# Kernel tuning notes

Measured on AMD Instinct MI355X. Metric: run time of the kernel, lower is better.

## Reference

```python
import jax, jax.numpy as jnp
import numpy as np

SIGMA = 1.0
LN2 = 0.6931471805599453


def _raster_mask(kd, kh, kw, include_center):
    # PixelCNN-style causal mask in (depth, h, w) raster order
    idx = np.arange(kd * kh * kw).reshape(kd, kh, kw)
    c = (kd * kh * kw) // 2
    m = (idx <= c) if include_center else (idx < c)
    return jnp.asarray(m, jnp.float32)[None, None]  # [1,1,kd,kh,kw] (OIDHW broadcast)


def _conv3d(x, w, b, padding):
    y = jax.lax.conv_general_dilated(x, w, (1, 1, 1), padding,
                                     dimension_numbers=('NCDHW', 'OIDHW', 'NCDHW'))
    return y + b[None, :, None, None, None]


def _quantize1d(x, centers):
    # distances of every element to every center: [..., L]
    d = (x[..., None] - centers) ** 2
    phi_soft = jax.nn.softmax(-SIGMA * d, axis=-1)
    qsoft = jnp.einsum('...l,l->...', phi_soft, centers)
    symbols = jnp.argmin(d, axis=-1)  # int32 hard assignment
    qhard = centers[symbols]
    return qsoft, qhard, symbols


def setup_inputs() -> dict:
    key = jax.random.key(0)
    ks = jax.random.split(key, 8)
    N, H, W, C = 4, 128, 128, 16
    K, L = 24, 6
    s = 0.05
    return {
        'x': jax.random.normal(ks[0], (N, H, W, C), jnp.float32),
        'centers': jax.random.uniform(ks[1], (L,), jnp.float32, -2.0, 2.0),
        'w0': jax.random.normal(ks[2], (K, 1, 3, 3, 3), jnp.float32) * s,
        'b0': jnp.zeros((K,), jnp.float32),
        'w1': jax.random.normal(ks[3], (K, K, 3, 3, 3), jnp.float32) * s,
        'b1': jnp.zeros((K,), jnp.float32),
        'w2': jax.random.normal(ks[4], (K, K, 3, 3, 3), jnp.float32) * s,
        'b2': jnp.zeros((K,), jnp.float32),
        'w_out': jax.random.normal(ks[5], (L, K, 1, 1, 1), jnp.float32) * s,
        'b_out': jnp.zeros((L,), jnp.float32),
    }


def reference(x, centers, w0, b0, w1, b1, w2, b2, w_out, b_out):
    # ---- soft/hard quantization with straight-through estimator ----
    qsoft, qhard, symbols = _quantize1d(x, centers)
    qbar = qsoft + jax.lax.stop_gradient(qhard - qsoft)  # [N,H,W,C] NHWC

    pc_in = jnp.transpose(qbar, (0, 3, 1, 2))[:, None]      # [N,1,C,H,W] (depth=C)
    tgt = jnp.transpose(symbols, (0, 3, 1, 2))              # [N,C,H,W]

    # pad input volume with pad_value = centers[0] (causal boundary symbol)
    pad_value = centers[0].astype(pc_in.dtype)
    v = jax.lax.pad(pc_in, pad_value,
                    [(0, 0, 0), (0, 0, 0), (1, 1, 0), (1, 1, 0), (1, 1, 0)])

    mask_a = _raster_mask(3, 3, 3, include_center=False)
    mask_b = _raster_mask(3, 3, 3, include_center=True)

    # res_shallow: masked-A conv -> masked-B conv -> masked-B conv + residual -> 1x1x1 logits
    h0 = jax.nn.relu(_conv3d(v, w0 * mask_a, b0, 'VALID'))     # [N,K,C,H,W]
    h1 = jax.nn.relu(_conv3d(h0, w1 * mask_b, b1, 'SAME'))
    h2 = _conv3d(h1, w2 * mask_b, b2, 'SAME') + h0
    logits = _conv3d(jax.nn.relu(h2), w_out, b_out, 'SAME')    # [N,L,C,H,W]

    # per-element bitcost: cross-entropy of hard symbols, in bits
    lp = jax.nn.log_softmax(logits, axis=1)
    bc = -jnp.take_along_axis(lp, tgt[:, None], axis=1)[:, 0] / LN2  # [N,C,H,W]
    bc_train = jnp.transpose(bc, (0, 2, 3, 1))                        # NCHW -> NHWC
    return qbar, bc_train
```

## Files before the change

kernel.cpp:

```cpp
#include <hip/hip_runtime.h>
#include <cstddef>

typedef _Float16 f16;
typedef _Float16 f16x8 __attribute__((ext_vector_type(8)));
typedef float f32x16 __attribute__((ext_vector_type(16)));

#define N_ 4
#define D_ 16
#define H_ 128
#define W_ 128
#define K_ 24
#define L_ 6
#define NTAP_A 13

#define OFF_Q    0ull
#define OFF_TGT  4194304ull
#define OFF_H0   8388608ull
#define OFF_H1   58720256ull
#define OFF_W0P  109051904ull
#define OFF_W1B  109053952ull
#define OFF_W2B  109075456ull

#define AROW_B 6336
#define A_HALVES 22176
#define B_HALVES 10752
#define E_HALVES 6144

__host__ __device__ constexpr int aoff(int p, int c, int g) {
  int idx8 = 2 * c + g;
  int ts = idx8 >= 3 ? 1 : 0;
  int t = 2 * p + ts;
  int cb = idx8 - 3 * ts;
  int dz = t / 9 - 1;
  int rr = t % 9;
  int dy = rr / 3 - 1;
  int dx = rr % 3 - 1;
  int rowb = (dz < 0) ? (dy + 1) : (4 + dy + 1);
  return rowb * AROW_B + (dx + 1) * 48 + cb * 16;
}

__global__ void pack_weights_k(const float* __restrict__ w0,
                               const float* __restrict__ w1,
                               const float* __restrict__ w2,
                               float* __restrict__ w0p,
                               f16* __restrict__ w1B,
                               f16* __restrict__ w2B) {
  int tid = threadIdx.x;
  for (int i = tid; i < NTAP_A * K_; i += 256) {
    int co = i % K_;
    int t  = i / K_;
    w0p[t * K_ + co] = w0[co * 27 + t];
  }
  for (int i = tid; i < 2 * B_HALVES; i += 256) {
    int sel = i / B_HALVES;
    int idx = i % B_HALVES;
    int chunk = idx / 512;
    int r = idx % 512;
    int g = r / 256;
    int n = (r % 256) / 8;
    int j = r % 8;
    int p = chunk / 3, c = chunk % 3;
    int idx8 = 2 * c + g;
    int ts = idx8 >= 3 ? 1 : 0;
    int t = 2 * p + ts;
    int ci = (idx8 - 3 * ts) * 8 + j;
    const float* w = sel ? w2 : w1;
    float v = (n < K_) ? w[(n * K_ + ci) * 27 + t] : 0.f;
    (sel ? w2B : w1B)[idx] = (f16)v;
  }
}

__global__ __launch_bounds__(256) void quantize_k(
    const float* __restrict__ x, const float* __restrict__ centers,
    float* __restrict__ qbar_out, float* __restrict__ q,
    int* __restrict__ tgt) {
  int idx = blockIdx.x * 256 + threadIdx.x;
  int w = idx & 127;
  int h = (idx >> 7) & 127;
  int c = (idx >> 14) & 15;
  int n = idx >> 18;

  float cs[L_];
#pragma unroll
  for (int l = 0; l < L_; ++l) cs[l] = centers[l];

  int xi = ((n * H_ + h) * W_ + w) * D_ + c;
  float xv = x[xi];

  float dv[L_];
  float dmin = 3.4e38f;
  int sym = 0;
#pragma unroll
  for (int l = 0; l < L_; ++l) {
    float df = xv - cs[l];
    float d = df * df;
    dv[l] = d;
    if (d < dmin) { dmin = d; sym = l; }
  }
  float e[L_];
  float s = 0.f;
#pragma unroll
  for (int l = 0; l < L_; ++l) {
    e[l] = expf(dmin - dv[l]);
    s += e[l];
  }
  float qsoft = 0.f;
#pragma unroll
  for (int l = 0; l < L_; ++l) qsoft += (e[l] / s) * cs[l];

  float qhard = cs[sym];
  float qb = qsoft + (qhard - qsoft);

  qbar_out[xi] = qb;
  q[idx] = qb;
  tgt[idx] = sym;
}

__global__ __launch_bounds__(256) void conv0_k(
    const float* __restrict__ q, const float* __restrict__ w0p,
    const float* __restrict__ b0, const float* __restrict__ centers,
    f16* __restrict__ h0) {
  float pv = centers[0];

  int blk = blockIdx.x;
  int h2 = blk & 63;
  int d = (blk >> 6) & 15;
  int n = blk >> 10;
  int w = threadIdx.x & 127;
  int h = (h2 << 1) | (threadIdx.x >> 7);

  float acc[K_];
#pragma unroll
  for (int i = 0; i < K_; ++i) acc[i] = b0[i];

  const float* base = q + ((n * D_ + d) * H_ + h) * W_ + w;

#pragma unroll 1
  for (int t = 0; t < NTAP_A; ++t) {
    int dz = t / 9 - 1;
    int r = t % 9;
    int dy = r / 3 - 1;
    int dx = r % 3 - 1;
    int hh = h + dy, ww = w + dx, dd = d + dz;
    bool ok = (dd >= 0) && ((unsigned)hh < H_) && ((unsigned)ww < W_);
    float xv = ok ? base[(dz * H_ + dy) * W_ + dx] : pv;
    const float* wr = w0p + t * K_;
#pragma unroll
    for (int co = 0; co < K_; ++co) acc[co] = fmaf(xv, wr[co], acc[co]);
  }

  union { f16 hv[24]; uint4 u[3]; } u;
#pragma unroll
  for (int i = 0; i < K_; ++i) u.hv[i] = (f16)fmaxf(acc[i], 0.f);
  size_t pos = (size_t)(((n * D_ + d) * H_ + h) * W_ + w);
  uint4* dst = (uint4*)(h0 + pos * K_);
  dst[0] = u.u[0]; dst[1] = u.u[1]; dst[2] = u.u[2];
}

__device__ __forceinline__ f32x16 conv_core(const f16* __restrict__ src,
                                            const f16* __restrict__ wB,
                                            f16* ldsA, f16* ldsB,
                                            int n, int d, int h_base) {
  const int tid = threadIdx.x;
  {
    const uint4* g = (const uint4*)wB;
    uint4* s = (uint4*)ldsB;
    for (int i = tid; i < 1344; i += 512) s[i] = g[i];
  }
#pragma unroll
  for (int it = 0; it < 6; ++it) {
    int i = it * 512 + tid;
    if (i < 2688) {
      int r = i / 384, qq = i % 384;
      int dd = (r < 4) ? d - 1 : d;
      int hh = h_base - 1 + ((r < 4) ? r : r - 4);
      uint4 v = make_uint4(0, 0, 0, 0);
      if (dd >= 0 && hh >= 0 && hh < H_) {
        const uint4* g = (const uint4*)(src + (size_t)((n * D_ + dd) * H_ + hh) * 3072);
        v = g[qq];
      }
      *(uint4*)((char*)ldsA + r * AROW_B + 48 + qq * 16) = v;
    }
  }
  if (tid < 42) {
    int r = tid / 6, k = tid % 6;
    int byte = r * AROW_B + (k < 3 ? k * 16 : 6192 + (k - 3) * 16);
    *(uint4*)((char*)ldsA + byte) = make_uint4(0, 0, 0, 0);
  }
  __syncthreads();

  const int lane = tid & 63;
  const int wv = tid >> 6;
  const int hs = wv >> 2;
  const int wbase = (wv & 3) * 32;
  const int m = lane & 31;
  const int g01 = lane >> 5;

  const char* Ab = (char*)ldsA + hs * AROW_B + (wbase + m) * 48;
  const char* Bb = (char*)ldsB + g01 * 512 + m * 16;

  f32x16 acc;
#pragma unroll
  for (int r = 0; r < 16; ++r) acc[r] = 0.f;

#pragma unroll
  for (int p = 0; p < 7; ++p) {
#pragma unroll
    for (int c = 0; c < 3; ++c) {
      constexpr int dummy = 0; (void)dummy;
      const int C0 = aoff(p, c, 0);
      const int C1 = aoff(p, c, 1);
      f16x8 a = *(const f16x8*)(Ab + (g01 ? C1 : C0));
      f16x8 b = *(const f16x8*)(Bb + (p * 3 + c) * 1024);
      acc = __builtin_amdgcn_mfma_f32_32x32x16_f16(a, b, acc, 0, 0, 0);
    }
  }
  return acc;
}

__global__ __launch_bounds__(512) void conv1_mfma_k(
    const f16* __restrict__ src, const f16* __restrict__ wB,
    const float* __restrict__ bias, f16* __restrict__ dst) {
  __shared__ f16 ldsA[A_HALVES];
  __shared__ f16 ldsB[B_HALVES];
  __shared__ f16 ldsE[E_HALVES];

  int blk = blockIdx.x;
  int hb = blk & 63;
  int d = (blk >> 6) & 15;
  int n = blk >> 10;
  int h_base = hb * 2;

  f32x16 acc = conv_core(src, wB, ldsA, ldsB, n, d, h_base);

  const int lane = threadIdx.x & 63;
  const int wv = threadIdx.x >> 6;
  const int hs = wv >> 2;
  const int wbase = (wv & 3) * 32;
  const int co = lane & 31;
  const int g01 = lane >> 5;

  if (co < K_) {
    float bv = bias[co];
#pragma unroll
    for (int r = 0; r < 16; ++r) {
      int mrow = (r & 3) + 8 * (r >> 2) + 4 * g01;
      int pos = hs * 128 + wbase + mrow;
      ldsE[pos * K_ + co] = (f16)fmaxf(acc[r] + bv, 0.f);
    }
  }
  __syncthreads();
  {
    uint4* g = (uint4*)(dst + (size_t)((n * D_ + d) * H_ + h_base) * 3072);
    const uint4* s = (const uint4*)ldsE;
    for (int i = threadIdx.x; i < 768; i += 512) g[i] = s[i];
  }
}

__global__ __launch_bounds__(512) void conv2_mfma_k(
    const f16* __restrict__ h1, const f16* __restrict__ h0,
    const f16* __restrict__ wB, const float* __restrict__ bias,
    const float* __restrict__ w_out, const float* __restrict__ b_out,
    const int* __restrict__ tgt, float* __restrict__ bco) {
  __shared__ f16 ldsA[A_HALVES];
  __shared__ f16 ldsB[B_HALVES];
  __shared__ f16 ldsE[E_HALVES];

  int blk = blockIdx.x;
  int hb = blk & 63;
  int d = (blk >> 6) & 15;
  int n = blk >> 10;
  int h_base = hb * 2;

  f32x16 acc = conv_core(h1, wB, ldsA, ldsB, n, d, h_base);

  {
    const uint4* g = (const uint4*)(h0 + (size_t)((n * D_ + d) * H_ + h_base) * 3072);
    uint4* s = (uint4*)ldsE;
    for (int i = threadIdx.x; i < 768; i += 512) s[i] = g[i];
  }
  __syncthreads();

  const int lane = threadIdx.x & 63;
  const int wv = threadIdx.x >> 6;
  const int hs = wv >> 2;
  const int wbase = (wv & 3) * 32;
  const int co = lane & 31;
  const int g01 = lane >> 5;

  if (co < K_) {
    float bv = bias[co];
#pragma unroll
    for (int r = 0; r < 16; ++r) {
      int mrow = (r & 3) + 8 * (r >> 2) + 4 * g01;
      int pos = hs * 128 + wbase + mrow;
      float h0v = (float)ldsE[pos * K_ + co];
      ldsE[pos * K_ + co] = (f16)fmaxf(acc[r] + bv + h0v, 0.f);
    }
  }
  __syncthreads();

  if (threadIdx.x < 256) {
    int pos = threadIdx.x;
    int hh = h_base + (pos >> 7);
    int w = pos & 127;

    const f16x8* ep = (const f16x8*)(ldsE + pos * K_);
    f16x8 e0 = ep[0], e1 = ep[1], e2 = ep[2];

    float lg[L_];
#pragma unroll
    for (int l = 0; l < L_; ++l) lg[l] = b_out[l];
#pragma unroll
    for (int k = 0; k < K_; ++k) {
      float rv = (float)(k < 8 ? e0[k] : (k < 16 ? e1[k - 8] : e2[k - 16]));
#pragma unroll
      for (int l = 0; l < L_; ++l) lg[l] = fmaf(rv, w_out[l * K_ + k], lg[l]);
    }
    float mm = lg[0];
#pragma unroll
    for (int l = 1; l < L_; ++l) mm = fmaxf(mm, lg[l]);
    float s = 0.f;
#pragma unroll
    for (int l = 0; l < L_; ++l) s += expf(lg[l] - mm);

    int t = tgt[((n * D_ + d) * H_ + hh) * W_ + w];
    float lt = lg[0];
#pragma unroll
    for (int l = 1; l < L_; ++l) lt = (t == l) ? lg[l] : lt;

    float lp = lt - mm - logf(s);
    bco[(size_t)((n * H_ + hh) * W_ + w) * D_ + d] = -lp / 0.69314718055994530942f;
  }
}

extern "C" void kernel_launch(void* const* d_in, const int* in_sizes, int n_in,
                              void* d_out, int out_size, void* d_ws, size_t ws_size,
                              hipStream_t stream) {
  const float* x       = (const float*)d_in[0];
  const float* centers = (const float*)d_in[1];
  const float* w0      = (const float*)d_in[2];
  const float* b0      = (const float*)d_in[3];
  const float* w1      = (const float*)d_in[4];
  const float* b1      = (const float*)d_in[5];
  const float* w2      = (const float*)d_in[6];
  const float* b2      = (const float*)d_in[7];
  const float* w_out   = (const float*)d_in[8];
  const float* b_out   = (const float*)d_in[9];
  float* out = (float*)d_out;

  char* ws = (char*)d_ws;
  float* q    = (float*)(ws + OFF_Q);
  int*   tg   = (int*)(ws + OFF_TGT);
  f16*   h0f  = (f16*)(ws + OFF_H0);
  f16*   h1f  = (f16*)(ws + OFF_H1);
  float* w0p  = (float*)(ws + OFF_W0P);
  f16*   w1B  = (f16*)(ws + OFF_W1B);
  f16*   w2B  = (f16*)(ws + OFF_W2B);

  hipLaunchKernelGGL(pack_weights_k, dim3(1), dim3(256), 0, stream,
                     w0, w1, w2, w0p, w1B, w2B);
  hipLaunchKernelGGL(quantize_k, dim3(4096), dim3(256), 0, stream,
                     x, centers, out, q, tg);
  hipLaunchKernelGGL(conv0_k, dim3(4096), dim3(256), 0, stream,
                     q, w0p, b0, centers, h0f);
  hipLaunchKernelGGL(conv1_mfma_k, dim3(4096), dim3(512), 0, stream,
                     h0f, w1B, b1, h1f);
  hipLaunchKernelGGL(conv2_mfma_k, dim3(4096), dim3(512), 0, stream,
                     h1f, h0f, w2B, b2, w_out, b_out, tg, out + 1048576);
}
```

Measured before the change: 220.0 us.

## Enlarge conv tiles to eight rows per block with two MFMA accumulators

```diff
diff --git a/kernel.cpp b/kernel.cpp
--- a/kernel.cpp
+++ b/kernel.cpp
@@ -22,9 +22,9 @@
 #define OFF_W2B  109075456ull
 
 #define AROW_B 6336
-#define A_HALVES 22176
-#define B_HALVES 10752
-#define E_HALVES 6144
+#define A_BYTES 120384
+#define B_BYTES 21504
+#define SMEM_BYTES 141888
 
 __host__ __device__ constexpr int aoff(int p, int c, int g) {
   int idx8 = 2 * c + g;
@@ -35,7 +35,7 @@
   int rr = t % 9;
   int dy = rr / 3 - 1;
   int dx = rr % 3 - 1;
-  int rowb = (dz < 0) ? (dy + 1) : (4 + dy + 1);
+  int rowb = (dz < 0) ? (dy + 1) : (10 + dy + 1);
   return rowb * AROW_B + (dx + 1) * 48 + cb * 16;
 }
 
@@ -45,15 +45,15 @@
                                float* __restrict__ w0p,
                                f16* __restrict__ w1B,
                                f16* __restrict__ w2B) {
-  int tid = threadIdx.x;
-  for (int i = tid; i < NTAP_A * K_; i += 256) {
+  int gid = blockIdx.x * 256 + threadIdx.x;
+  for (int i = gid; i < NTAP_A * K_; i += 2048) {
     int co = i % K_;
     int t  = i / K_;
     w0p[t * K_ + co] = w0[co * 27 + t];
   }
-  for (int i = tid; i < 2 * B_HALVES; i += 256) {
-    int sel = i / B_HALVES;
-    int idx = i % B_HALVES;
+  for (int i = gid; i < 2 * 10752; i += 2048) {
+    int sel = i / 10752;
+    int idx = i % 10752;
     int chunk = idx / 512;
     int r = idx % 512;
     int g = r / 256;
@@ -157,163 +157,165 @@
   dst[0] = u.u[0]; dst[1] = u.u[1]; dst[2] = u.u[2];
 }
 
-__device__ __forceinline__ f32x16 conv_core(const f16* __restrict__ src,
-                                            const f16* __restrict__ wB,
-                                            f16* ldsA, f16* ldsB,
-                                            int n, int d, int h_base) {
+__device__ __forceinline__ void conv_core8(const f16* __restrict__ src,
+                                           const f16* __restrict__ wB,
+                                           char* smem, int n, int d, int h_base,
+                                           f32x16& acc0, f32x16& acc1) {
   const int tid = threadIdx.x;
+  for (int i = tid; i < 7296; i += 1024) {
+    int r = i / 384, qq = i % 384;
+    int dd = (r < 10) ? d - 1 : d;
+    int hh = h_base - 1 + ((r < 10) ? r : r - 10);
+    uint4 v = make_uint4(0, 0, 0, 0);
+    if (dd >= 0 && (unsigned)hh < (unsigned)H_)
+      v = ((const uint4*)(src + (size_t)((n * D_ + dd) * H_ + hh) * 3072))[qq];
+    *(uint4*)(smem + r * AROW_B + 48 + qq * 16) = v;
+  }
+  if (tid < 114) {
+    int r = tid / 6, k = tid % 6;
+    int byte = r * AROW_B + (k < 3 ? k * 16 : 6192 + (k - 3) * 16);
+    *(uint4*)(smem + byte) = make_uint4(0, 0, 0, 0);
+  }
   {
     const uint4* g = (const uint4*)wB;
-    uint4* s = (uint4*)ldsB;
-    for (int i = tid; i < 1344; i += 512) s[i] = g[i];
-  }
-#pragma unroll
-  for (int it = 0; it < 6; ++it) {
-    int i = it * 512 + tid;
-    if (i < 2688) {
-      int r = i / 384, qq = i % 384;
-      int dd = (r < 4) ? d - 1 : d;
-      int hh = h_base - 1 + ((r < 4) ? r : r - 4);
-      uint4 v = make_uint4(0, 0, 0, 0);
-      if (dd >= 0 && hh >= 0 && hh < H_) {
-        const uint4* g = (const uint4*)(src + (size_t)((n * D_ + dd) * H_ + hh) * 3072);
-        v = g[qq];
-      }
-      *(uint4*)((char*)ldsA + r * AROW_B + 48 + qq * 16) = v;
-    }
-  }
-  if (tid < 42) {
-    int r = tid / 6, k = tid % 6;
-    int byte = r * AROW_B + (k < 3 ? k * 16 : 6192 + (k - 3) * 16);
-    *(uint4*)((char*)ldsA + byte) = make_uint4(0, 0, 0, 0);
+    uint4* s = (uint4*)(smem + A_BYTES);
+    for (int i = tid; i < 1344; i += 1024) s[i] = g[i];
   }
   __syncthreads();
 
   const int lane = tid & 63;
   const int wv = tid >> 6;
-  const int hs = wv >> 2;
-  const int wbase = (wv & 3) * 32;
   const int m = lane & 31;
   const int g01 = lane >> 5;
 
-  const char* Ab = (char*)ldsA + hs * AROW_B + (wbase + m) * 48;
-  const char* Bb = (char*)ldsB + g01 * 512 + m * 16;
-
-  f32x16 acc;
-#pragma unroll
-  for (int r = 0; r < 16; ++r) acc[r] = 0.f;
+  const int hs = wv >> 1;
+  const int wc0 = (wv & 1) * 64;
+  const char* Ab0 = smem + hs * AROW_B + (wc0 + m) * 48;
+  const char* Ab1 = Ab0 + 32 * 48;
+  const char* Bb = smem + A_BYTES + g01 * 512 + m * 16;
+
+#pragma unroll
+  for (int r = 0; r < 16; ++r) { acc0[r] = 0.f; acc1[r] = 0.f; }
 
 #pragma unroll
   for (int p = 0; p < 7; ++p) {
 #pragma unroll
     for (int c = 0; c < 3; ++c) {
-      constexpr int dummy = 0; (void)dummy;
       const int C0 = aoff(p, c, 0);
       const int C1 = aoff(p, c, 1);
-      f16x8 a = *(const f16x8*)(Ab + (g01 ? C1 : C0));
+      int off = g01 ? C1 : C0;
       f16x8 b = *(const f16x8*)(Bb + (p * 3 + c) * 1024);
-      acc = __builtin_amdgcn_mfma_f32_32x32x16_f16(a, b, acc, 0, 0, 0);
-    }
-  }
-  return acc;
-}
-
-__global__ __launch_bounds__(512) void conv1_mfma_k(
+      f16x8 a0 = *(const f16x8*)(Ab0 + off);
+      f16x8 a1 = *(const f16x8*)(Ab1 + off);
+      acc0 = __builtin_amdgcn_mfma_f32_32x32x16_f16(a0, b, acc0, 0, 0, 0);
+      acc1 = __builtin_amdgcn_mfma_f32_32x32x16_f16(a1, b, acc1, 0, 0, 0);
+    }
+  }
+}
+
+__global__ __launch_bounds__(1024, 1) void conv1_mfma_k(
     const f16* __restrict__ src, const f16* __restrict__ wB,
     const float* __restrict__ bias, f16* __restrict__ dst) {
-  __shared__ f16 ldsA[A_HALVES];
-  __shared__ f16 ldsB[B_HALVES];
-  __shared__ f16 ldsE[E_HALVES];
+  __shared__ __align__(16) char smem[SMEM_BYTES];
 
   int blk = blockIdx.x;
-  int hb = blk & 63;
-  int d = (blk >> 6) & 15;
-  int n = blk >> 10;
-  int h_base = hb * 2;
-
-  f32x16 acc = conv_core(src, wB, ldsA, ldsB, n, d, h_base);
+  int hb = blk & 15;
+  int d = (blk >> 4) & 15;
+  int n = blk >> 8;
+  int h_base = hb * 8;
+
+  f32x16 acc0, acc1;
+  conv_core8(src, wB, smem, n, d, h_base, acc0, acc1);
 
   const int lane = threadIdx.x & 63;
   const int wv = threadIdx.x >> 6;
-  const int hs = wv >> 2;
-  const int wbase = (wv & 3) * 32;
-  const int co = lane & 31;
+  const int m = lane & 31;
   const int g01 = lane >> 5;
 
-  if (co < K_) {
-    float bv = bias[co];
-#pragma unroll
-    for (int r = 0; r < 16; ++r) {
-      int mrow = (r & 3) + 8 * (r >> 2) + 4 * g01;
-      int pos = hs * 128 + wbase + mrow;
-      ldsE[pos * K_ + co] = (f16)fmaxf(acc[r] + bv, 0.f);
+  __syncthreads();
+  f16* ldsE = (f16*)smem;
+  if (m < K_) {
+    float bv = bias[m];
+#pragma unroll
+    for (int tt = 0; tt < 2; ++tt) {
+      const f32x16& A = tt ? acc1 : acc0;
+#pragma unroll
+      for (int r = 0; r < 16; ++r) {
+        int mrow = (r & 3) + 8 * (r >> 2) + 4 * g01;
+        int pos = (2 * wv + tt) * 32 + mrow;
+        ldsE[pos * K_ + m] = (f16)fmaxf(A[r] + bv, 0.f);
+      }
     }
   }
   __syncthreads();
   {
     uint4* g = (uint4*)(dst + (size_t)((n * D_ + d) * H_ + h_base) * 3072);
-    const uint4* s = (const uint4*)ldsE;
-    for (int i = threadIdx.x; i < 768; i += 512) g[i] = s[i];
-  }
-}
-
-__global__ __launch_bounds__(512) void conv2_mfma_k(
+    const uint4* s = (const uint4*)smem;
+    for (int i = threadIdx.x; i < 3072; i += 1024) g[i] = s[i];
+  }
+}
+
+__global__ __launch_bounds__(1024, 1) void conv2_mfma_k(
     const f16* __restrict__ h1, const f16* __restrict__ h0,
     const f16* __restrict__ wB, const float* __restrict__ bias,
     const float* __restrict__ w_out, const float* __restrict__ b_out,
     const int* __restrict__ tgt, float* __restrict__ bco) {
-  __shared__ f16 ldsA[A_HALVES];
-  __shared__ f16 ldsB[B_HALVES];
-  __shared__ f16 ldsE[E_HALVES];
+  __shared__ __align__(16) char smem[SMEM_BYTES];
 
   int blk = blockIdx.x;
-  int hb = blk & 63;
-  int d = (blk >> 6) & 15;
-  int n = blk >> 10;
-  int h_base = hb * 2;
-
-  f32x16 acc = conv_core(h1, wB, ldsA, ldsB, n, d, h_base);
-
-  {
-    const uint4* g = (const uint4*)(h0 + (size_t)((n * D_ + d) * H_ + h_base) * 3072);
-    uint4* s = (uint4*)ldsE;
-    for (int i = threadIdx.x; i < 768; i += 512) s[i] = g[i];
-  }
-  __syncthreads();
+  int hb = blk & 15;
+  int d = (blk >> 4) & 15;
+  int n = blk >> 8;
+  int h_base = hb * 8;
+
+  f32x16 acc0, acc1;
+  conv_core8(h1, wB, smem, n, d, h_base, acc0, acc1);
 
   const int lane = threadIdx.x & 63;
   const int wv = threadIdx.x >> 6;
-  const int hs = wv >> 2;
-  const int wbase = (wv & 3) * 32;
-  const int co = lane & 31;
+  const int m = lane & 31;
   const int g01 = lane >> 5;
 
-  if (co < K_) {
-    float bv = bias[co];
-#pragma unroll
-    for (int r = 0; r < 16; ++r) {
-      int mrow = (r & 3) + 8 * (r >> 2) + 4 * g01;
-      int pos = hs * 128 + wbase + mrow;
-      float h0v = (float)ldsE[pos * K_ + co];
-      ldsE[pos * K_ + co] = (f16)fmaxf(acc[r] + bv + h0v, 0.f);
-    }
-  }
-  __syncthreads();
-
-  if (threadIdx.x < 256) {
+  __syncthreads();
+  float* Ef = (float*)smem;
+  if (m < K_) {
+    float bv = bias[m];
+#pragma unroll
+    for (int tt = 0; tt < 2; ++tt) {
+      const f32x16& A = tt ? acc1 : acc0;
+#pragma unroll
+      for (int r = 0; r < 16; ++r) {
+        int mrow = (r & 3) + 8 * (r >> 2) + 4 * g01;
+        int pos = (2 * wv + tt) * 32 + mrow;
+        Ef[pos * 28 + m] = A[r] + bv;
+      }
+    }
+  }
+  __syncthreads();
+
+  {
     int pos = threadIdx.x;
     int hh = h_base + (pos >> 7);
     int w = pos & 127;
 
-    const f16x8* ep = (const f16x8*)(ldsE + pos * K_);
-    f16x8 e0 = ep[0], e1 = ep[1], e2 = ep[2];
+    size_t gpos = (size_t)((n * D_ + d) * H_ + h_base) * W_ + pos;
+    const f16x8* hp = (const f16x8*)(h0 + gpos * K_);
+    f16x8 e0 = hp[0], e1 = hp[1], e2 = hp[2];
+
+    const float* ef = Ef + pos * 28;
+    float vals[K_];
+#pragma unroll
+    for (int k = 0; k < K_; ++k) {
+      float h0v = (float)(k < 8 ? e0[k] : (k < 16 ? e1[k - 8] : e2[k - 16]));
+      vals[k] = fmaxf(ef[k] + h0v, 0.f);
+    }
 
     float lg[L_];
 #pragma unroll
     for (int l = 0; l < L_; ++l) lg[l] = b_out[l];
 #pragma unroll
     for (int k = 0; k < K_; ++k) {
-      float rv = (float)(k < 8 ? e0[k] : (k < 16 ? e1[k - 8] : e2[k - 16]));
+      float rv = vals[k];
 #pragma unroll
       for (int l = 0; l < L_; ++l) lg[l] = fmaf(rv, w_out[l * K_ + k], lg[l]);
     }
@@ -324,7 +326,7 @@
 #pragma unroll
     for (int l = 0; l < L_; ++l) s += expf(lg[l] - mm);
 
-    int t = tgt[((n * D_ + d) * H_ + hh) * W_ + w];
+    int t = tgt[gpos];
     float lt = lg[0];
 #pragma unroll
     for (int l = 1; l < L_; ++l) lt = (t == l) ? lg[l] : lt;
@@ -358,14 +360,14 @@
   f16*   w1B  = (f16*)(ws + OFF_W1B);
   f16*   w2B  = (f16*)(ws + OFF_W2B);
 
-  hipLaunchKernelGGL(pack_weights_k, dim3(1), dim3(256), 0, stream,
+  hipLaunchKernelGGL(pack_weights_k, dim3(8), dim3(256), 0, stream,
                      w0, w1, w2, w0p, w1B, w2B);
   hipLaunchKernelGGL(quantize_k, dim3(4096), dim3(256), 0, stream,
                      x, centers, out, q, tg);
   hipLaunchKernelGGL(conv0_k, dim3(4096), dim3(256), 0, stream,
                      q, w0p, b0, centers, h0f);
-  hipLaunchKernelGGL(conv1_mfma_k, dim3(4096), dim3(512), 0, stream,
+  hipLaunchKernelGGL(conv1_mfma_k, dim3(1024), dim3(1024), 0, stream,
                      h0f, w1B, b1, h1f);
-  hipLaunchKernelGGL(conv2_mfma_k, dim3(4096), dim3(512), 0, stream,
+  hipLaunchKernelGGL(conv2_mfma_k, dim3(1024), dim3(1024), 0, stream,
                      h1f, h0f, w2B, b2, w_out, b_out, tg, out + 1048576);
 }
```

New measurement: 197.7 us. 1.11x faster.
